# Kernel optimization log

Hardware: AMD Instinct MI355X
Metric: run time of the kernel (lower is better)

Reference implementation:

```python
import jax, jax.numpy as jnp
import numpy as np

MARGIN = 70.0
THR = 125.0
PD_EPS = 1e-6  # torch F.pairwise_distance default eps


def _return_cam(features, weight_softmax, class_idx):
    # features: [bz, nc, h, w]; weight_softmax: [n_cls, nc]; class_idx: [bz]
    w_sel = weight_softmax[class_idx]                     # [bz, nc]
    cam = jnp.einsum('bc,bchw->bhw', w_sel, features)     # [bz, h, w]
    cam = cam - cam.min(axis=(1, 2), keepdims=True)
    cam = cam / cam.max(axis=(1, 2), keepdims=True) * 255.0
    return cam[:, None]                                   # [bz, 1, h, w]


def _pairwise_distance(x, y):
    # torch F.pairwise_distance: ||x - y + eps||_2 along last dim
    return jnp.sqrt(jnp.sum((x - y + PD_EPS) ** 2, axis=-1))


def setup_inputs() -> dict:
    key = jax.random.key(0)
    ks = jax.random.split(key, 6)
    bz, nc, h, w, n_cls = 64, 2048, 14, 14, 1000
    return {
        'pred': jax.random.normal(ks[0], (bz, n_cls), jnp.float32),
        'cla_truth': jax.random.randint(ks[1], (bz,), 0, n_cls, jnp.int32),
        'seg_truth': jax.random.uniform(ks[2], (bz, h, w), jnp.float32),
        'features_blobs': jax.random.normal(ks[3], (bz, nc, h, w), jnp.float32),
        'weight_softmax': jax.random.normal(ks[4], (n_cls, nc), jnp.float32),
        'idx': jax.random.randint(ks[5], (bz, 3), 0, n_cls, jnp.int32),
    }


def reference(pred, cla_truth, seg_truth, features_blobs, weight_softmax, idx):
    bz, nc, h, w = features_blobs.shape
    # cross entropy
    logp = jax.nn.log_softmax(pred, axis=-1)
    loss1 = -jnp.mean(logp[jnp.arange(bz), cla_truth])
    # CAMs for top-3 predicted classes
    cam0 = _return_cam(features_blobs, weight_softmax, idx[:, 0])  # [bz,1,h,w]
    cam1 = _return_cam(features_blobs, weight_softmax, idx[:, 1])
    cam2 = _return_cam(features_blobs, weight_softmax, idx[:, 2])
    # binarize cam0 (values in [0,255]); <=thr -> 0, >thr -> 1
    dst = jnp.where(cam0[:, 0] > THR, 1.0, 0.0)                     # [bz,h,w]
    # row-wise distance to seg truth, averaged over rows
    ed1 = jnp.mean(_pairwise_distance(dst, seg_truth), axis=1)      # [bz]
    # CAM-weighted features via broadcasted matmul (requires h == w)
    fea0 = jnp.matmul(cam0, features_blobs)                         # [bz,nc,h,w]
    fea1 = jnp.matmul(cam1, features_blobs)
    fea2 = jnp.matmul(cam2, features_blobs)
    d01 = _pairwise_distance(fea0.reshape(bz, -1), fea1.reshape(bz, -1)) / nc
    d02 = _pairwise_distance(fea0.reshape(bz, -1), fea2.reshape(bz, -1)) / nc
    loss_dis = jnp.mean(ed1 + jnp.clip(MARGIN - d01 - d02, 0.0, None)) + loss1
    return loss_dis
```

## Files before the change

kernel.cpp:

```cpp
#include <hip/hip_runtime.h>
#include <math.h>

#define BZ      64
#define NC      2048
#define HH      14
#define HW      196
#define NCLS    1000
#define SPLITS  8
#define CPB     (NC/SPLITS)
#define CHUNK   8
#define NCHUNK  (CPB/CHUNK)
#define LPAD    200
#define NTRI    105
#define KSPL    53

#define CAM_OFF  0
#define G_OFF    (BZ*SPLITS*3*HW)
#define S_OFF    (G_OFF + BZ*SPLITS*HW)
#define CE_OFF   (S_OFF + BZ*SPLITS*HH)
#define TICK_OFF (CE_OFF + BZ)

template<int MODE>
__device__ __forceinline__ float bred(float v, float* red){
  #pragma unroll
  for (int o=32;o>0;o>>=1){
    float u = __shfl_down(v, o, 64);
    if (MODE==0) v += u; else if (MODE==1) v = fminf(v,u); else v = fmaxf(v,u);
  }
  __syncthreads();
  if ((threadIdx.x & 63)==0) red[threadIdx.x>>6] = v;
  __syncthreads();
  float r = red[0];
  #pragma unroll
  for (int w=1;w<4;w++){
    float u = red[w];
    if (MODE==0) r += u; else if (MODE==1) r = fminf(r,u); else r = fmaxf(r,u);
  }
  return r;
}

template<int LO, int HI>
__device__ __forceinline__ void gramStep(const float* __restrict__ colp,
                                         float* __restrict__ acc){
  float x[14];
  #pragma unroll
  for (int m=0;m<14;m++) x[m] = colp[m*HH];
  #pragma unroll
  for (int m=0;m<14;m++){
    #pragma unroll
    for (int n=m;n<14;n++){
      const int k = 14*m - (m*(m-1))/2 + (n-m);
      if (k >= LO && k < HI) acc[k-LO] += x[m]*x[n];
    }
  }
}

__global__ __launch_bounds__(256) void k_init(
    const float* __restrict__ pred, const int* __restrict__ cla,
    float* __restrict__ ws)
{
  const int t = threadIdx.x, b = blockIdx.x;
  __shared__ float red[4];
  if (t == 0) ((int*)ws)[TICK_OFF + b] = 0;

  const float* pb = pred + (size_t)b*NCLS;
  float mv = -3.0e38f;
  for (int i=t;i<NCLS;i+=256) mv = fmaxf(mv, pb[i]);
  mv = bred<2>(mv, red);
  float es = 0.f;
  for (int i=t;i<NCLS;i+=256) es += expf(pb[i]-mv);
  es = bred<0>(es, red);
  if (t==0){
    float lse = mv + logf(es);
    ws[CE_OFF + b] = lse - pb[cla[b]];
  }
}

__global__ __launch_bounds__(256, 2) void k_main(
    const float* __restrict__ F, const float* __restrict__ W,
    const int* __restrict__ idx, const float* __restrict__ seg,
    float* __restrict__ ws, float* __restrict__ out)
{
  __shared__ __align__(16) float Fs[2][CHUNK*LPAD];
  __shared__ __align__(16) float wls[3][CPB];
  __shared__ __align__(16) float sred[HW];
  __shared__ int lastFlag;
  __shared__ __align__(16) union Ovl {
    float gacc[224*KSPL];
    struct {
      float cam[3][HW]; float Gt[NTRI]; float Sv[HH];
      float D1[HW]; float D2[HW]; float EE[HW];
      float rowv[HH]; float dc1[HH]; float dc2[HH];
      float red[4]; float scal[6];
    } p2;
  } U;

  const int t = threadIdx.x;
  const int s = blockIdx.x;
  const int b = blockIdx.y;
  const int cbase = s*CPB;

  const int gteam = (t < 112) ? 0 : ((t >= 128 && t < 240) ? 1 : -1);
  const int cc    = (t < 128) ? t : (t - 128);
  const int cL    = cc & 7;
  const int jc    = cc >> 3;
  const bool isCam = (t < 196);
  const bool isLd  = (t < 196);

  {
    const int i0 = idx[b*3+0], i1 = idx[b*3+1], i2 = idx[b*3+2];
    wls[0][t] = W[(size_t)i0*NC + cbase + t];
    wls[1][t] = W[(size_t)i1*NC + cbase + t];
    wls[2][t] = W[(size_t)i2*NC + cbase + t];

    const float4* Fb4 = (const float4*)(F + ((size_t)b*NC + cbase)*HW);

    float acc[KSPL];
    #pragma unroll
    for (int k=0;k<KSPL;k++) acc[k]=0.f;
    float cam0=0.f, cam1=0.f, cam2=0.f, ssum=0.f;

    float4 p0, p1;
    auto loadChunk = [&](int ch){
      if (isLd){
        const float4* src = Fb4 + (size_t)ch*392;
        p0 = src[2*t]; p1 = src[2*t+1];
      }
    };
    auto storeChunk = [&](int bufi){
      if (isLd){
        float4* dst = (float4*)(&Fs[bufi][0]);
        int i = 2*t;   dst[(i/49)*(LPAD/4) + (i%49)] = p0;
        i = 2*t+1;     dst[(i/49)*(LPAD/4) + (i%49)] = p1;
      }
    };

    loadChunk(0);
    storeChunk(0);
    __syncthreads();

    #pragma unroll 1
    for (int ch = 0; ch < NCHUNK; ++ch){
      const int bufi = ch & 1;
      if (ch+1 < NCHUNK) loadChunk(ch+1);
      const float* Fsb = &Fs[bufi][0];

      if (gteam == 0){
        gramStep<0,KSPL>(Fsb + cL*LPAD + jc, acc);
      } else if (gteam == 1){
        gramStep<KSPL,NTRI>(Fsb + cL*LPAD + jc, acc);
      }
      if (isCam){
        float w0a[CHUNK], w1a[CHUNK], w2a[CHUNK];
        *(float4*)&w0a[0] = *(const float4*)&wls[0][ch*CHUNK];
        *(float4*)&w0a[4] = *(const float4*)&wls[0][ch*CHUNK+4];
        *(float4*)&w1a[0] = *(const float4*)&wls[1][ch*CHUNK];
        *(float4*)&w1a[4] = *(const float4*)&wls[1][ch*CHUNK+4];
        *(float4*)&w2a[0] = *(const float4*)&wls[2][ch*CHUNK];
        *(float4*)&w2a[4] = *(const float4*)&wls[2][ch*CHUNK+4];
        #pragma unroll
        for (int c=0;c<CHUNK;c++){
          float v = Fsb[c*LPAD + t];
          cam0 += w0a[c]*v; cam1 += w1a[c]*v; cam2 += w2a[c]*v; ssum += v;
        }
      }
      if (ch+1 < NCHUNK) storeChunk((ch+1)&1);
      __syncthreads();
    }

    const size_t pslot = (size_t)(b*SPLITS + s);
    if (isCam){
      float* base = ws + CAM_OFF + pslot*3*HW;
      base[t]        = cam0;
      base[HW + t]   = cam1;
      base[2*HW + t] = cam2;
      sred[t] = ssum;
    }
    if (gteam == 0){
      float* gr = &U.gacc[(size_t)cc*KSPL];
      #pragma unroll
      for (int k=0;k<KSPL;k++) gr[k] = acc[k];
    } else if (gteam == 1){
      float* gr = &U.gacc[(size_t)(112+cc)*KSPL];
      #pragma unroll
      for (int k=0;k<NTRI-KSPL;k++) gr[k] = acc[k];
    }
    __syncthreads();

    if (t < NTRI){
      float a = 0.f;
      if (t < KSPL){
        for (int r=0; r<112; r++)   a += U.gacc[(size_t)r*KSPL + t];
      } else {
        for (int r=112; r<224; r++) a += U.gacc[(size_t)r*KSPL + (t-KSPL)];
      }
      ws[G_OFF + pslot*HW + t] = a;
    }
    if (t >= 128 && t < 128+HH){
      int r = t - 128;
      float a = 0.f;
      #pragma unroll
      for (int j=0;j<HH;j++) a += sred[r*HH+j];
      ws[S_OFF + pslot*HH + r] = a;
    }
    __syncthreads();
  }

  if (t == 0){
    __threadfence();
    int old = atomicAdd(&((int*)ws)[TICK_OFF + b], 1);
    lastFlag = (old == SPLITS-1) ? 1 : 0;
    __threadfence();
  }
  __syncthreads();

  if (lastFlag){
    volatile const float* vws = (volatile const float*)ws;

    if (t < HW){
      for (int k=0;k<3;k++){
        float a=0.f;
        for (int sp=0;sp<SPLITS;sp++)
          a += vws[CAM_OFF + ((size_t)(b*SPLITS+sp)*3 + k)*HW + t];
        U.p2.cam[k][t]=a;
      }
    }
    if (t < NTRI){
      float g=0.f;
      for (int sp=0;sp<SPLITS;sp++) g += vws[G_OFF + (size_t)(b*SPLITS+sp)*HW + t];
      U.p2.Gt[t]=g;
    }
    if (t < HH){
      float a=0.f;
      for (int sp=0;sp<SPLITS;sp++) a += vws[S_OFF + (size_t)(b*SPLITS+sp)*HH + t];
      U.p2.Sv[t]=a;
    }
    __syncthreads();

    for (int k=0;k<3;k++){
      float v = (t<HW)? U.p2.cam[k][t] : 3.0e38f;
      float mn = bred<1>(v, U.p2.red);
      v = (t<HW)? U.p2.cam[k][t] : -3.0e38f;
      float mx = bred<2>(v, U.p2.red);
      if (t==0){ U.p2.scal[2*k]=mn; U.p2.scal[2*k+1]=mx; }
    }
    __syncthreads();

    if (t < HW){
      float c0 = (U.p2.cam[0][t]-U.p2.scal[0]) / (U.p2.scal[1]-U.p2.scal[0]) * 255.0f;
      float c1 = (U.p2.cam[1][t]-U.p2.scal[2]) / (U.p2.scal[3]-U.p2.scal[2]) * 255.0f;
      float c2 = (U.p2.cam[2][t]-U.p2.scal[4]) / (U.p2.scal[5]-U.p2.scal[4]) * 255.0f;
      float dst = (c0 > 125.0f) ? 1.0f : 0.0f;
      U.p2.D1[t] = c0 - c1; U.p2.D2[t] = c0 - c2;
      float e = dst - seg[(size_t)b*HW + t] + 1e-6f;
      U.p2.EE[t] = e*e;
    }
    __syncthreads();

    if (t < HH){
      float rs=0.f, d1=0.f, d2=0.f;
      #pragma unroll
      for (int j=0;j<HH;j++){
        rs += U.p2.EE[t*HH+j];
        d1 += U.p2.D1[j*HH+t];
        d2 += U.p2.D2[j*HH+t];
      }
      U.p2.rowv[t] = sqrtf(rs); U.p2.dc1[t]=d1; U.p2.dc2[t]=d2;
    }
    __syncthreads();

    float v1=0.f, v2=0.f;
    if (t < HW){
      int m = t/HH, mp = t%HH;
      float h1=0.f, h2=0.f;
      #pragma unroll
      for (int i=0;i<HH;i++){
        h1 += U.p2.D1[i*HH+m]*U.p2.D1[i*HH+mp];
        h2 += U.p2.D2[i*HH+m]*U.p2.D2[i*HH+mp];
      }
      int mm = (m<mp)?m:mp, nn = (m<mp)?mp:m;
      float g = U.p2.Gt[14*mm - (mm*(mm-1))/2 + (nn-mm)];
      v1 = h1*g; v2 = h2*g;
    }
    float sx2_1 = bred<0>(v1, U.p2.red);
    float sx2_2 = bred<0>(v2, U.p2.red);

    if (t==0){
      float ce = vws[CE_OFF + b];
      float ed1 = 0.f;
      #pragma unroll
      for (int i=0;i<HH;i++) ed1 += U.p2.rowv[i];
      ed1 *= (1.0f/14.0f);
      float sx1=0.f, sx2=0.f;
      #pragma unroll
      for (int m=0;m<HH;m++){ sx1 += U.p2.dc1[m]*U.p2.Sv[m]; sx2 += U.p2.dc2[m]*U.p2.Sv[m]; }
      const float NEPS2 = 401408.0f * 1e-12f;
      float d01 = sqrtf(sx2_1 + 2e-6f*sx1 + NEPS2) * (1.0f/2048.0f);
      float d02 = sqrtf(sx2_2 + 2e-6f*sx2 + NEPS2) * (1.0f/2048.0f);
      float term = ed1 + fmaxf(0.0f, 70.0f - d01 - d02) + ce;
      atomicAdd(out, term * (1.0f/64.0f));
    }
  }
}

extern "C" void kernel_launch(void* const* d_in, const int* in_sizes, int n_in,
                              void* d_out, int out_size, void* d_ws, size_t ws_size,
                              hipStream_t stream) {
  const float* pred = (const float*)d_in[0];
  const int*   cla  = (const int*)  d_in[1];
  const float* seg  = (const float*)d_in[2];
  const float* F    = (const float*)d_in[3];
  const float* W    = (const float*)d_in[4];
  const int*   idx  = (const int*)  d_in[5];
  float* out = (float*)d_out;
  float* ws  = (float*)d_ws;

  k_init<<<BZ, 256, 0, stream>>>(pred, cla, ws);
  k_main<<<dim3(SPLITS, BZ), 256, 0, stream>>>(F, W, idx, seg, ws, out);
}
```

Measured before the change: 207.3 us.

## Double the channel splits, shrink LDS via wave-shuffle Gram reduction, deepen prefetch

The channel splits per batch are doubled, giving twice as many blocks, and the launch-bounds occupancy target rises from 2 to 4 blocks per CU. The large per-thread Gram-accumulator staging array in LDS is replaced by a cross-lane shuffle reduction plus a tiny per-wave buffer. The feature tiles now overlay the phase-2 scratch, which cuts shared memory enough to fit more blocks per CU. Global loads are prefetched two chunks ahead through alternating register sets. The trade-offs are many extra shuffle instructions for 53 accumulators, more partial results for the last block to combine, and extra register pressure under the tighter launch bound.

```diff
diff --git a/kernel.cpp b/kernel.cpp
--- a/kernel.cpp
+++ b/kernel.cpp
@@ -6,7 +6,7 @@
 #define HH      14
 #define HW      196
 #define NCLS    1000
-#define SPLITS  8
+#define SPLITS  16
 #define CPB     (NC/SPLITS)
 #define CHUNK   8
 #define NCHUNK  (CPB/CHUNK)
@@ -76,17 +76,13 @@
   }
 }
 
-__global__ __launch_bounds__(256, 2) void k_main(
+__global__ __launch_bounds__(256, 4) void k_main(
     const float* __restrict__ F, const float* __restrict__ W,
     const int* __restrict__ idx, const float* __restrict__ seg,
     float* __restrict__ ws, float* __restrict__ out)
 {
-  __shared__ __align__(16) float Fs[2][CHUNK*LPAD];
-  __shared__ __align__(16) float wls[3][CPB];
-  __shared__ __align__(16) float sred[HW];
-  __shared__ int lastFlag;
   __shared__ __align__(16) union Ovl {
-    float gacc[224*KSPL];
+    float Fs[2][CHUNK*LPAD];
     struct {
       float cam[3][HW]; float Gt[NTRI]; float Sv[HH];
       float D1[HW]; float D2[HW]; float EE[HW];
@@ -94,6 +90,10 @@
       float red[4]; float scal[6];
     } p2;
   } U;
+  __shared__ __align__(16) float wls[3][CPB];
+  __shared__ __align__(16) float sred[HW];
+  __shared__ __align__(16) float gred[4][KSPL];
+  __shared__ int lastFlag;
 
   const int t = threadIdx.x;
   const int s = blockIdx.x;
@@ -107,43 +107,48 @@
   const bool isCam = (t < 196);
   const bool isLd  = (t < 196);
 
+  float acc[KSPL];
+  #pragma unroll
+  for (int k=0;k<KSPL;k++) acc[k]=0.f;
+
   {
     const int i0 = idx[b*3+0], i1 = idx[b*3+1], i2 = idx[b*3+2];
-    wls[0][t] = W[(size_t)i0*NC + cbase + t];
-    wls[1][t] = W[(size_t)i1*NC + cbase + t];
-    wls[2][t] = W[(size_t)i2*NC + cbase + t];
+    if (t < CPB){
+      wls[0][t] = W[(size_t)i0*NC + cbase + t];
+      wls[1][t] = W[(size_t)i1*NC + cbase + t];
+      wls[2][t] = W[(size_t)i2*NC + cbase + t];
+    }
 
     const float4* Fb4 = (const float4*)(F + ((size_t)b*NC + cbase)*HW);
 
-    float acc[KSPL];
-    #pragma unroll
-    for (int k=0;k<KSPL;k++) acc[k]=0.f;
     float cam0=0.f, cam1=0.f, cam2=0.f, ssum=0.f;
 
-    float4 p0, p1;
-    auto loadChunk = [&](int ch){
+    float4 qA0, qA1, qB0, qB1;
+    auto loadTo = [&](int ch, float4& x0, float4& x1){
       if (isLd){
         const float4* src = Fb4 + (size_t)ch*392;
-        p0 = src[2*t]; p1 = src[2*t+1];
+        x0 = src[2*t]; x1 = src[2*t+1];
       }
     };
-    auto storeChunk = [&](int bufi){
+    auto storeFrom = [&](int bufi, const float4& x0, const float4& x1){
       if (isLd){
-        float4* dst = (float4*)(&Fs[bufi][0]);
-        int i = 2*t;   dst[(i/49)*(LPAD/4) + (i%49)] = p0;
-        i = 2*t+1;     dst[(i/49)*(LPAD/4) + (i%49)] = p1;
+        float4* dst = (float4*)(&U.Fs[bufi][0]);
+        int i = 2*t;   dst[(i/49)*(LPAD/4) + (i%49)] = x0;
+        i = 2*t+1;     dst[(i/49)*(LPAD/4) + (i%49)] = x1;
       }
     };
 
-    loadChunk(0);
-    storeChunk(0);
+    loadTo(0, qA0, qA1);
+    storeFrom(0, qA0, qA1);
+    loadTo(1, qB0, qB1);
     __syncthreads();
 
     #pragma unroll 1
     for (int ch = 0; ch < NCHUNK; ++ch){
-      const int bufi = ch & 1;
-      if (ch+1 < NCHUNK) loadChunk(ch+1);
-      const float* Fsb = &Fs[bufi][0];
+      if (ch+2 < NCHUNK){
+        if ((ch&1)==0) loadTo(ch+2, qA0, qA1); else loadTo(ch+2, qB0, qB1);
+      }
+      const float* Fsb = &U.Fs[ch&1][0];
 
       if (gteam == 0){
         gramStep<0,KSPL>(Fsb + cL*LPAD + jc, acc);
@@ -151,20 +156,19 @@
         gramStep<KSPL,NTRI>(Fsb + cL*LPAD + jc, acc);
       }
       if (isCam){
-        float w0a[CHUNK], w1a[CHUNK], w2a[CHUNK];
-        *(float4*)&w0a[0] = *(const float4*)&wls[0][ch*CHUNK];
-        *(float4*)&w0a[4] = *(const float4*)&wls[0][ch*CHUNK+4];
-        *(float4*)&w1a[0] = *(const float4*)&wls[1][ch*CHUNK];
-        *(float4*)&w1a[4] = *(const float4*)&wls[1][ch*CHUNK+4];
-        *(float4*)&w2a[0] = *(const float4*)&wls[2][ch*CHUNK];
-        *(float4*)&w2a[4] = *(const float4*)&wls[2][ch*CHUNK+4];
         #pragma unroll
         for (int c=0;c<CHUNK;c++){
-          float v = Fsb[c*LPAD + t];
-          cam0 += w0a[c]*v; cam1 += w1a[c]*v; cam2 += w2a[c]*v; ssum += v;
+          float w0 = wls[0][ch*CHUNK+c];
+          float w1 = wls[1][ch*CHUNK+c];
+          float w2 = wls[2][ch*CHUNK+c];
+          float v  = Fsb[c*LPAD + t];
+          cam0 += w0*v; cam1 += w1*v; cam2 += w2*v; ssum += v;
         }
       }
-      if (ch+1 < NCHUNK) storeChunk((ch+1)&1);
+      if (ch+1 < NCHUNK){
+        if ((ch&1)==0) storeFrom((ch+1)&1, qB0, qB1);
+        else           storeFrom((ch+1)&1, qA0, qA1);
+      }
       __syncthreads();
     }
 
@@ -176,24 +180,22 @@
       base[2*HW + t] = cam2;
       sred[t] = ssum;
     }
-    if (gteam == 0){
-      float* gr = &U.gacc[(size_t)cc*KSPL];
-      #pragma unroll
-      for (int k=0;k<KSPL;k++) gr[k] = acc[k];
-    } else if (gteam == 1){
-      float* gr = &U.gacc[(size_t)(112+cc)*KSPL];
-      #pragma unroll
-      for (int k=0;k<NTRI-KSPL;k++) gr[k] = acc[k];
+
+    #pragma unroll
+    for (int o=32;o>0;o>>=1){
+      #pragma unroll
+      for (int k=0;k<KSPL;k++) acc[k] += __shfl_xor(acc[k], o, 64);
+    }
+    const int wv = t >> 6;
+    if ((t & 63)==0){
+      #pragma unroll
+      for (int k=0;k<KSPL;k++) gred[wv][k] = acc[k];
     }
     __syncthreads();
 
     if (t < NTRI){
-      float a = 0.f;
-      if (t < KSPL){
-        for (int r=0; r<112; r++)   a += U.gacc[(size_t)r*KSPL + t];
-      } else {
-        for (int r=112; r<224; r++) a += U.gacc[(size_t)r*KSPL + (t-KSPL)];
-      }
+      float a = (t < KSPL) ? (gred[0][t] + gred[1][t])
+                           : (gred[2][t-KSPL] + gred[3][t-KSPL]);
       ws[G_OFF + pslot*HW + t] = a;
     }
     if (t >= 128 && t < 128+HH){
```

Measured after the change: 244.6 us. +18.0%, slower.
